# Performance work log

Hardware: AMD Instinct MI355X
Metric: run time of the kernel (lower is better)

The kernel has to match this reference:

```python
import jax, jax.numpy as jnp
import numpy as np

HEADS = 16
HEAD_DIM = 64  # embed_size 1024 // 16


def setup_inputs() -> dict:
    key = jax.random.key(0)
    ks = jax.random.split(key, 6)
    N, S, E = 2, 2048, 1024
    return {
        "values": jax.random.normal(ks[0], (N, S, E), dtype=jnp.float32),
        "keys": jax.random.normal(ks[1], (N, S, E), dtype=jnp.float32),
        "queries": jax.random.normal(ks[2], (N, S, E), dtype=jnp.float32),
        "Wv": jax.random.normal(ks[3], (E, E), dtype=jnp.float32) * (E ** -0.5),
        "Wk": jax.random.normal(ks[4], (E, E), dtype=jnp.float32) * (E ** -0.5),
        "Wq": jax.random.normal(ks[5], (E, E), dtype=jnp.float32) * (E ** -0.5),
    }


def reference(values, keys, queries, Wv, Wk, Wq):
    N, Sq, E = queries.shape
    Sk = keys.shape[1]
    H, D = HEADS, HEAD_DIM
    # linear projections (torch Linear: x @ W^T), then split heads
    v = (values @ Wv.T).reshape(N, Sk, H, D)
    k = (keys @ Wk.T).reshape(N, Sk, H, D)
    q = (queries @ Wq.T).reshape(N, Sq, H, D)
    # QK^T -> [N, H, Q, K]
    scores = jnp.einsum("nqhd,nkhd->nhqk", q, k)
    # no mask (original forward takes mask=None path); scale by sqrt(head_dim)
    attn = jax.nn.softmax(scores / jnp.asarray(D, scores.dtype) ** 0.5, axis=-1)
    # AV -> [N, Q, H, D] -> [N, Q, E]; note: fc_out is never applied in the original forward
    out = jnp.einsum("nhql,nlhd->nqhd", attn, v).reshape(N, Sq, H * D)
    return out
```

## Files before the change

kernel.cpp:

```cpp
#include <hip/hip_runtime.h>
#include <math.h>

#define SEQ 2048
#define EMB 1024
#define NH  16
#define HD  64

typedef __attribute__((ext_vector_type(8))) short short8;
typedef __attribute__((ext_vector_type(4))) float f32x4;

static const size_t XE = (size_t)2 * SEQ * EMB;
static const size_t WE = (size_t)EMB * EMB;

static __device__ __forceinline__ short f2bf(float f) {
    unsigned u = __builtin_bit_cast(unsigned, f);
    u = u + 0x7fffu + ((u >> 16) & 1u);
    return (short)(u >> 16);
}

#if __has_builtin(__builtin_amdgcn_cvt_pk_bf16_f32)
typedef __attribute__((ext_vector_type(2))) __bf16 bf16x2;
static __device__ __forceinline__ unsigned pk2(float a, float b) {
    bf16x2 v = __builtin_amdgcn_cvt_pk_bf16_f32(a, b);
    return __builtin_bit_cast(unsigned, v);
}
#else
static __device__ __forceinline__ unsigned pk2(float a, float b) {
    return (unsigned)(unsigned short)f2bf(a) |
           ((unsigned)(unsigned short)f2bf(b) << 16);
}
#endif

static __device__ __forceinline__ short8 cvt8(float4 a, float4 b) {
    union { unsigned u[4]; short8 s; } r;
    r.u[0] = pk2(a.x, a.y); r.u[1] = pk2(a.z, a.w);
    r.u[2] = pk2(b.x, b.y); r.u[3] = pk2(b.z, b.w);
    return r.s;
}

static __device__ __forceinline__ void gload16(const void* g, void* l) {
    __builtin_amdgcn_global_load_lds(
        (const __attribute__((address_space(1))) void*)g,
        (__attribute__((address_space(3))) void*)l, 16, 0, 0);
}

__global__ __launch_bounds__(256)
void cvt_all(const float* __restrict__ xq, const float* __restrict__ xk,
             const float* __restrict__ xv, const float* __restrict__ wq,
             const float* __restrict__ wk, const float* __restrict__ wv,
             short* __restrict__ dxq, short* __restrict__ dxk,
             short* __restrict__ dxv, short* __restrict__ dw) {
    int id = blockIdx.x;
    const float* s; short* d; size_t i;
    if (id < 6144) {
        int seg = id >> 11, o = id & 2047;
        s = (seg == 0) ? xq : (seg == 1) ? xk : xv;
        d = (seg == 0) ? dxq : (seg == 1) ? dxk : dxv;
        i = (size_t)o * 256 + threadIdx.x;
    } else {
        int wid = id - 6144;
        int seg = wid >> 9, o = wid & 511;
        s = (seg == 0) ? wq : (seg == 1) ? wk : wv;
        d = dw + (size_t)seg * WE;
        i = (size_t)o * 256 + threadIdx.x;
    }
    const float4* sp = (const float4*)s;
    float4 a = sp[2 * i], b = sp[2 * i + 1];
    *(short8*)(d + i * 8) = cvt8(a, b);
}

#define ES_STRIDE 136
__global__ __launch_bounds__(512, 4)
void proj(const short* __restrict__ Xq, const short* __restrict__ Xk,
          const short* __restrict__ Xv, const short* __restrict__ Wb,
          short* __restrict__ qb, short* __restrict__ kbuf,
          short* __restrict__ vt) {
    __shared__ __align__(16) char lds_raw[65536];
    short8* Fs = (short8*)lds_raw;
    short8* Hs = (short8*)(lds_raw + 32768);
    short*  Es = (short*)lds_raw;

    const int L = blockIdx.x;
    const int xcd = L & 7, i = L >> 3;
    const int z = i >> 5;
    const int m = i & 31;
    const int ty = xcd * 4 + (m & 3);
    const int tx = m >> 2;

    const short* Fop; const short* Hop; short* C;
    if (z == 0)      { Fop = Xq; Hop = Wb;           C = qb;   }
    else if (z == 1) { Fop = Xk; Hop = Wb + WE;      C = kbuf; }
    else             { Fop = Xv; Hop = Wb + 2 * WE;  C = vt;   }
    const int fr0 = ty * 128;
    const int hr0 = tx * 128;

    const int t = threadIdx.x, w = t >> 6, lane = t & 63;
    const int l15 = lane & 15, quad = lane >> 4;
    const int lr3 = lane >> 3, lc7 = lane & 7;
    const int mh = (w >> 2) * 64;
    const int nh = (w & 3) * 32;

    auto stageF = [&](int pp, int k0) {
#pragma unroll
        for (int j = 0; j < 2; ++j) {
            int rb = j * 64 + w * 8;
            gload16(Fop + (size_t)(fr0 + rb + lr3) * EMB + k0 + ((lc7 ^ lr3) * 8),
                    &Fs[pp * 1024 + rb * 8]);
        }
    };
    auto stageH = [&](int pp, int k0) {
#pragma unroll
        for (int j = 0; j < 2; ++j) {
            int rb = j * 64 + w * 8;
            gload16(Hop + (size_t)(hr0 + rb + lr3) * EMB + k0 + ((lc7 ^ lr3) * 8),
                    &Hs[pp * 1024 + rb * 8]);
        }
    };

    f32x4 acc[4][2];
#pragma unroll
    for (int a = 0; a < 4; ++a)
#pragma unroll
        for (int b = 0; b < 2; ++b) acc[a][b] = 0.f;

    stageF(0, 0);
    stageH(0, 0);

    int p = 0;
    for (int k0 = 0; k0 < EMB; k0 += 64, p ^= 1) {
        __syncthreads();
        if (k0 + 64 < EMB) { stageF(p ^ 1, k0 + 64); stageH(p ^ 1, k0 + 64); }

#pragma unroll
        for (int kb2 = 0; kb2 < 2; ++kb2) {
            short8 af[4], bf[2];
            int cx = (kb2 * 4 + quad) ^ (l15 & 7);
            if (z < 2) {
#pragma unroll
                for (int mi = 0; mi < 4; ++mi)
                    af[mi] = Fs[p * 1024 + (mh + mi * 16 + l15) * 8 + cx];
#pragma unroll
                for (int ni = 0; ni < 2; ++ni)
                    bf[ni] = Hs[p * 1024 + (nh + ni * 16 + l15) * 8 + cx];
            } else {
#pragma unroll
                for (int mi = 0; mi < 4; ++mi)
                    af[mi] = Hs[p * 1024 + (mh + mi * 16 + l15) * 8 + cx];
#pragma unroll
                for (int ni = 0; ni < 2; ++ni)
                    bf[ni] = Fs[p * 1024 + (nh + ni * 16 + l15) * 8 + cx];
            }
#pragma unroll
            for (int mi = 0; mi < 4; ++mi)
#pragma unroll
                for (int ni = 0; ni < 2; ++ni)
                    acc[mi][ni] = __builtin_amdgcn_mfma_f32_16x16x32_bf16(
                        af[mi], bf[ni], acc[mi][ni], 0, 0, 0);
        }
    }

    __syncthreads();
#pragma unroll
    for (int mi = 0; mi < 4; ++mi)
#pragma unroll
        for (int ni = 0; ni < 2; ++ni)
#pragma unroll
            for (int r = 0; r < 4; ++r) {
                int lr_ = mh + mi * 16 + quad * 4 + r;
                int lc_ = nh + ni * 16 + l15;
                Es[lr_ * ES_STRIDE + lc_] = f2bf(acc[mi][ni][r]);
            }
    __syncthreads();
    {
        int row = t >> 2, q4 = t & 3;
        const short* src = Es + row * ES_STRIDE + q4 * 32;
        short* dst;
        if (z < 2) {
            dst = C + (size_t)(fr0 + row) * EMB + hr0 + q4 * 32;
        } else {
            int bz = fr0 >> 11, s0 = fr0 & 2047;
            dst = C + ((size_t)bz * EMB + hr0 + row) * SEQ + s0 + q4 * 32;
        }
#pragma unroll
        for (int j = 0; j < 4; ++j)
            *(short8*)(dst + j * 8) = *(const short8*)(src + j * 8);
    }
}

__global__ __launch_bounds__(256, 2)
void attn_mfma(const short* __restrict__ Qg, const short* __restrict__ Kg,
               const short* __restrict__ Vtg, float* __restrict__ OutD) {
    __shared__ short8 QPs[1024];
    __shared__ short8 Ks[2][1024];
    __shared__ short8 Vs[2][1024];

    const int t = threadIdx.x, w = t >> 6, lane = t & 63;
    const int l15 = lane & 15, quad = lane >> 4;
    const int lr3 = lane >> 3, lc7 = lane & 7;
    const int L = blockIdx.x;
    const int xcd = L & 7, i = L >> 3;
    const int bh = xcd * 4 + (i & 3);
    const int q0 = (i >> 2) * 128;
    const int b = bh >> 4, h = bh & 15;
    const short* Qb = Qg + (size_t)b * SEQ * EMB + h * HD;
    const short* Kb = Kg + (size_t)b * SEQ * EMB + h * HD;
    const short* Vb = Vtg + ((size_t)b * EMB + h * HD) * SEQ;

    auto stageKV = [&](int p, int kt) {
#pragma unroll
        for (int j = 0; j < 4; ++j) {
            int rb = w * 32 + j * 8;
            int krow = rb + lr3;
            gload16(Kb + (size_t)(kt + krow) * EMB + ((lc7 ^ (krow & 7)) * 8),
                    &Ks[p][rb * 8]);
            int half = w >> 1, db = (w & 1) * 32 + j * 8;
            int d = db + lr3;
            gload16(Vb + (size_t)d * SEQ + kt + half * 64 + ((lc7 ^ (d & 7)) * 8),
                    &Vs[p][half * 512 + db * 8]);
        }
    };

#pragma unroll
    for (int j = 0; j < 4; ++j) {
        int rb = w * 32 + j * 8;
        int row = rb + lr3;
        gload16(Qb + (size_t)(q0 + row) * EMB + ((lc7 ^ (row & 7)) * 8),
                &QPs[rb * 8]);
    }
    stageKV(0, 0);
    __syncthreads();

    short8 qf[2][2];
#pragma unroll
    for (int qi = 0; qi < 2; ++qi)
#pragma unroll
        for (int kb2 = 0; kb2 < 2; ++kb2) {
            int row = w * 32 + qi * 16 + l15;
            qf[qi][kb2] = QPs[row * 8 + ((kb2 * 4 + quad) ^ (l15 & 7))];
        }

    f32x4 o[2][4];
    float lr[2] = {0.f, 0.f};
#pragma unroll
    for (int qi = 0; qi < 2; ++qi)
#pragma unroll
        for (int ni = 0; ni < 4; ++ni) o[qi][ni] = 0.f;
    const float cl2 = 0.18033688011112042f;
    const float c0  = 11.541560327111707f;

    int p = 0;
    for (int kt = 0; kt < SEQ; kt += 128, p ^= 1) {
        if (kt) __syncthreads();
        if (kt + 128 < SEQ) stageKV(p ^ 1, kt + 128);

#pragma unroll
        for (int half = 0; half < 2; ++half) {
            f32x4 s[4][2];
#pragma unroll
            for (int kblk = 0; kblk < 4; ++kblk)
#pragma unroll
                for (int qi = 0; qi < 2; ++qi) s[kblk][qi] = 0.f;
#pragma unroll
            for (int kb2 = 0; kb2 < 2; ++kb2) {
                short8 ak[4];
#pragma unroll
                for (int kblk = 0; kblk < 4; ++kblk) {
                    int row = half * 64 + kblk * 16 + l15;
                    ak[kblk] = Ks[p][row * 8 + ((kb2 * 4 + quad) ^ (l15 & 7))];
                }
#pragma unroll
                for (int kblk = 0; kblk < 4; ++kblk)
#pragma unroll
                    for (int qi = 0; qi < 2; ++qi)
                        s[kblk][qi] = __builtin_amdgcn_mfma_f32_16x16x32_bf16(
                            ak[kblk], qf[qi][kb2], s[kblk][qi], 0, 0, 0);
            }

#pragma unroll
            for (int qi = 0; qi < 2; ++qi) {
                int row = w * 32 + qi * 16 + l15;
#pragma unroll
                for (int kblk = 0; kblk < 4; ++kblk) {
                    float p0 = __builtin_amdgcn_exp2f(fmaf(s[kblk][qi][0], cl2, -c0));
                    float p1 = __builtin_amdgcn_exp2f(fmaf(s[kblk][qi][1], cl2, -c0));
                    float p2 = __builtin_amdgcn_exp2f(fmaf(s[kblk][qi][2], cl2, -c0));
                    float p3 = __builtin_amdgcn_exp2f(fmaf(s[kblk][qi][3], cl2, -c0));
                    lr[qi] += (p0 + p1) + (p2 + p3);
                    uint2 pv; pv.x = pk2(p0, p1); pv.y = pk2(p2, p3);
                    int kc = kblk * 2 + (quad >> 1);
                    *(uint2*)((char*)QPs +
                        (((row * 8 + (kc ^ (l15 & 7))) << 4) | ((quad & 1) << 3)))
                        = pv;
                }
            }

#pragma unroll
            for (int kb2 = 0; kb2 < 2; ++kb2) {
                short8 ap[2], bv[4];
#pragma unroll
                for (int qi = 0; qi < 2; ++qi) {
                    int row = w * 32 + qi * 16 + l15;
                    ap[qi] = QPs[row * 8 + ((kb2 * 4 + quad) ^ (l15 & 7))];
                }
#pragma unroll
                for (int ni = 0; ni < 4; ++ni) {
                    int dr = ni * 16 + l15;
                    bv[ni] = Vs[p][half * 512 + dr * 8 +
                                   ((kb2 * 4 + quad) ^ (l15 & 7))];
                }
#pragma unroll
                for (int qi = 0; qi < 2; ++qi)
#pragma unroll
                    for (int ni = 0; ni < 4; ++ni)
                        o[qi][ni] = __builtin_amdgcn_mfma_f32_16x16x32_bf16(
                            ap[qi], bv[ni], o[qi][ni], 0, 0, 0);
            }
        }
    }

#pragma unroll
    for (int qi = 0; qi < 2; ++qi) {
        float l = lr[qi];
        l += __shfl_xor(l, 16);
        l += __shfl_xor(l, 32);
        lr[qi] = l;
    }
#pragma unroll
    for (int qi = 0; qi < 2; ++qi)
#pragma unroll
        for (int r = 0; r < 4; ++r) {
            float inv = 1.0f / __shfl(lr[qi], quad * 4 + r);
            int q = q0 + w * 32 + qi * 16 + quad * 4 + r;
            float* op = OutD + ((size_t)b * SEQ + q) * EMB + h * HD;
#pragma unroll
            for (int ni = 0; ni < 4; ++ni)
                op[ni * 16 + l15] = o[qi][ni][r] * inv;
        }
}

extern "C" void kernel_launch(void* const* d_in, const int* in_sizes, int n_in,
                              void* d_out, int out_size, void* d_ws, size_t ws_size,
                              hipStream_t stream) {
    const float* values  = (const float*)d_in[0];
    const float* keys    = (const float*)d_in[1];
    const float* queries = (const float*)d_in[2];
    const float* Wv      = (const float*)d_in[3];
    const float* Wk      = (const float*)d_in[4];
    const float* Wq      = (const float*)d_in[5];
    float* out = (float*)d_out;

    short* qb  = (short*)d_ws;
    short* kb  = qb + XE;
    short* vt  = kb + XE;
    short* wb  = vt + XE;
    short* xqb = wb + 3 * WE;
    short* xkb = xqb + XE;
    short* xvb = xkb + XE;

    cvt_all<<<7680, 256, 0, stream>>>(queries, keys, values, Wq, Wk, Wv,
                                      xqb, xkb, xvb, wb);
    proj<<<768, 512, 0, stream>>>(xqb, xkb, xvb, wb, qb, kb, vt);
    attn_mfma<<<512, 256, 0, stream>>>(qb, kb, vt, out);
}
```

Measured before the change: 188.9 us.

## Use 8 waves of 16 query rows with 64-key tiles in attention

Restructures the attention kernel to 512-thread blocks where each wave handles 16 query rows instead of 32, and shrinks the K/V tile from 128 to 64 keys, halving shared memory. This is meant to cut register and LDS footprint, raising occupancy and latency hiding. In exchange each K/V fragment loaded from LDS feeds half as many MFMAs, and there are twice as many barriers per key sequence.

```diff
diff --git a/kernel.cpp b/kernel.cpp
--- a/kernel.cpp
+++ b/kernel.cpp
@@ -187,12 +187,12 @@
     }
 }
 
-__global__ __launch_bounds__(256, 2)
+__global__ __launch_bounds__(512, 4)
 void attn_mfma(const short* __restrict__ Qg, const short* __restrict__ Kg,
                const short* __restrict__ Vtg, float* __restrict__ OutD) {
     __shared__ short8 QPs[1024];
-    __shared__ short8 Ks[2][1024];
-    __shared__ short8 Vs[2][1024];
+    __shared__ short8 Ks[2][512];
+    __shared__ short8 Vs[2][512];
 
     const int t = threadIdx.x, w = t >> 6, lane = t & 63;
     const int l15 = lane & 15, quad = lane >> 4;
@@ -207,135 +207,104 @@
     const short* Vb = Vtg + ((size_t)b * EMB + h * HD) * SEQ;
 
     auto stageKV = [&](int p, int kt) {
-#pragma unroll
-        for (int j = 0; j < 4; ++j) {
-            int rb = w * 32 + j * 8;
-            int krow = rb + lr3;
-            gload16(Kb + (size_t)(kt + krow) * EMB + ((lc7 ^ (krow & 7)) * 8),
-                    &Ks[p][rb * 8]);
-            int half = w >> 1, db = (w & 1) * 32 + j * 8;
-            int d = db + lr3;
-            gload16(Vb + (size_t)d * SEQ + kt + half * 64 + ((lc7 ^ (d & 7)) * 8),
-                    &Vs[p][half * 512 + db * 8]);
-        }
+        int krow = w * 8 + lr3;
+        gload16(Kb + (size_t)(kt + krow) * EMB + ((lc7 ^ lr3) * 8),
+                &Ks[p][w * 64]);
+        gload16(Vb + (size_t)krow * SEQ + kt + ((lc7 ^ lr3) * 8),
+                &Vs[p][w * 64]);
     };
 
 #pragma unroll
-    for (int j = 0; j < 4; ++j) {
-        int rb = w * 32 + j * 8;
+    for (int j = 0; j < 2; ++j) {
+        int rb = w * 16 + j * 8;
         int row = rb + lr3;
-        gload16(Qb + (size_t)(q0 + row) * EMB + ((lc7 ^ (row & 7)) * 8),
+        gload16(Qb + (size_t)(q0 + row) * EMB + ((lc7 ^ lr3) * 8),
                 &QPs[rb * 8]);
     }
     stageKV(0, 0);
     __syncthreads();
 
-    short8 qf[2][2];
-#pragma unroll
-    for (int qi = 0; qi < 2; ++qi)
-#pragma unroll
-        for (int kb2 = 0; kb2 < 2; ++kb2) {
-            int row = w * 32 + qi * 16 + l15;
-            qf[qi][kb2] = QPs[row * 8 + ((kb2 * 4 + quad) ^ (l15 & 7))];
-        }
-
-    f32x4 o[2][4];
-    float lr[2] = {0.f, 0.f};
-#pragma unroll
-    for (int qi = 0; qi < 2; ++qi)
-#pragma unroll
-        for (int ni = 0; ni < 4; ++ni) o[qi][ni] = 0.f;
+    short8 qf[2];
+#pragma unroll
+    for (int kb2 = 0; kb2 < 2; ++kb2) {
+        int row = w * 16 + l15;
+        qf[kb2] = QPs[row * 8 + ((kb2 * 4 + quad) ^ (l15 & 7))];
+    }
+
+    f32x4 o[4];
+    float lr = 0.f;
+#pragma unroll
+    for (int ni = 0; ni < 4; ++ni) o[ni] = 0.f;
     const float cl2 = 0.18033688011112042f;
     const float c0  = 11.541560327111707f;
 
     int p = 0;
-    for (int kt = 0; kt < SEQ; kt += 128, p ^= 1) {
+    for (int kt = 0; kt < SEQ; kt += 64, p ^= 1) {
         if (kt) __syncthreads();
-        if (kt + 128 < SEQ) stageKV(p ^ 1, kt + 128);
-
-#pragma unroll
-        for (int half = 0; half < 2; ++half) {
-            f32x4 s[4][2];
+        if (kt + 64 < SEQ) stageKV(p ^ 1, kt + 64);
+
+        f32x4 s[4];
+#pragma unroll
+        for (int kblk = 0; kblk < 4; ++kblk) s[kblk] = 0.f;
+#pragma unroll
+        for (int kb2 = 0; kb2 < 2; ++kb2) {
+            short8 ak[4];
+#pragma unroll
+            for (int kblk = 0; kblk < 4; ++kblk) {
+                int row = kblk * 16 + l15;
+                ak[kblk] = Ks[p][row * 8 + ((kb2 * 4 + quad) ^ (l15 & 7))];
+            }
 #pragma unroll
             for (int kblk = 0; kblk < 4; ++kblk)
-#pragma unroll
-                for (int qi = 0; qi < 2; ++qi) s[kblk][qi] = 0.f;
-#pragma unroll
-            for (int kb2 = 0; kb2 < 2; ++kb2) {
-                short8 ak[4];
-#pragma unroll
-                for (int kblk = 0; kblk < 4; ++kblk) {
-                    int row = half * 64 + kblk * 16 + l15;
-                    ak[kblk] = Ks[p][row * 8 + ((kb2 * 4 + quad) ^ (l15 & 7))];
-                }
-#pragma unroll
-                for (int kblk = 0; kblk < 4; ++kblk)
-#pragma unroll
-                    for (int qi = 0; qi < 2; ++qi)
-                        s[kblk][qi] = __builtin_amdgcn_mfma_f32_16x16x32_bf16(
-                            ak[kblk], qf[qi][kb2], s[kblk][qi], 0, 0, 0);
-            }
-
-#pragma unroll
-            for (int qi = 0; qi < 2; ++qi) {
-                int row = w * 32 + qi * 16 + l15;
-#pragma unroll
-                for (int kblk = 0; kblk < 4; ++kblk) {
-                    float p0 = __builtin_amdgcn_exp2f(fmaf(s[kblk][qi][0], cl2, -c0));
-                    float p1 = __builtin_amdgcn_exp2f(fmaf(s[kblk][qi][1], cl2, -c0));
-                    float p2 = __builtin_amdgcn_exp2f(fmaf(s[kblk][qi][2], cl2, -c0));
-                    float p3 = __builtin_amdgcn_exp2f(fmaf(s[kblk][qi][3], cl2, -c0));
-                    lr[qi] += (p0 + p1) + (p2 + p3);
-                    uint2 pv; pv.x = pk2(p0, p1); pv.y = pk2(p2, p3);
-                    int kc = kblk * 2 + (quad >> 1);
-                    *(uint2*)((char*)QPs +
-                        (((row * 8 + (kc ^ (l15 & 7))) << 4) | ((quad & 1) << 3)))
-                        = pv;
-                }
-            }
-
-#pragma unroll
-            for (int kb2 = 0; kb2 < 2; ++kb2) {
-                short8 ap[2], bv[4];
-#pragma unroll
-                for (int qi = 0; qi < 2; ++qi) {
-                    int row = w * 32 + qi * 16 + l15;
-                    ap[qi] = QPs[row * 8 + ((kb2 * 4 + quad) ^ (l15 & 7))];
-                }
-#pragma unroll
-                for (int ni = 0; ni < 4; ++ni) {
-                    int dr = ni * 16 + l15;
-                    bv[ni] = Vs[p][half * 512 + dr * 8 +
-                                   ((kb2 * 4 + quad) ^ (l15 & 7))];
-                }
-#pragma unroll
-                for (int qi = 0; qi < 2; ++qi)
-#pragma unroll
-                    for (int ni = 0; ni < 4; ++ni)
-                        o[qi][ni] = __builtin_amdgcn_mfma_f32_16x16x32_bf16(
-                            ap[qi], bv[ni], o[qi][ni], 0, 0, 0);
-            }
-        }
-    }
-
-#pragma unroll
-    for (int qi = 0; qi < 2; ++qi) {
-        float l = lr[qi];
-        l += __shfl_xor(l, 16);
-        l += __shfl_xor(l, 32);
-        lr[qi] = l;
-    }
-#pragma unroll
-    for (int qi = 0; qi < 2; ++qi)
-#pragma unroll
-        for (int r = 0; r < 4; ++r) {
-            float inv = 1.0f / __shfl(lr[qi], quad * 4 + r);
-            int q = q0 + w * 32 + qi * 16 + quad * 4 + r;
-            float* op = OutD + ((size_t)b * SEQ + q) * EMB + h * HD;
+                s[kblk] = __builtin_amdgcn_mfma_f32_16x16x32_bf16(
+                    ak[kblk], qf[kb2], s[kblk], 0, 0, 0);
+        }
+
+        {
+            int row = w * 16 + l15;
+#pragma unroll
+            for (int kblk = 0; kblk < 4; ++kblk) {
+                float p0 = __builtin_amdgcn_exp2f(fmaf(s[kblk][0], cl2, -c0));
+                float p1 = __builtin_amdgcn_exp2f(fmaf(s[kblk][1], cl2, -c0));
+                float p2 = __builtin_amdgcn_exp2f(fmaf(s[kblk][2], cl2, -c0));
+                float p3 = __builtin_amdgcn_exp2f(fmaf(s[kblk][3], cl2, -c0));
+                lr += (p0 + p1) + (p2 + p3);
+                uint2 pv; pv.x = pk2(p0, p1); pv.y = pk2(p2, p3);
+                int kc = kblk * 2 + (quad >> 1);
+                *(uint2*)((char*)QPs +
+                    (((row * 8 + (kc ^ (l15 & 7))) << 4) | ((quad & 1) << 3)))
+                    = pv;
+            }
+        }
+
+#pragma unroll
+        for (int kb2 = 0; kb2 < 2; ++kb2) {
+            int row = w * 16 + l15;
+            short8 ap = QPs[row * 8 + ((kb2 * 4 + quad) ^ (l15 & 7))];
+            short8 bv[4];
+#pragma unroll
+            for (int ni = 0; ni < 4; ++ni) {
+                int dr = ni * 16 + l15;
+                bv[ni] = Vs[p][dr * 8 + ((kb2 * 4 + quad) ^ (l15 & 7))];
+            }
 #pragma unroll
             for (int ni = 0; ni < 4; ++ni)
-                op[ni * 16 + l15] = o[qi][ni][r] * inv;
-        }
+                o[ni] = __builtin_amdgcn_mfma_f32_16x16x32_bf16(
+                    ap, bv[ni], o[ni], 0, 0, 0);
+        }
+    }
+
+    lr += __shfl_xor(lr, 16);
+    lr += __shfl_xor(lr, 32);
+#pragma unroll
+    for (int r = 0; r < 4; ++r) {
+        float inv = 1.0f / __shfl(lr, quad * 4 + r);
+        int q = q0 + w * 16 + quad * 4 + r;
+        float* op = OutD + ((size_t)b * SEQ + q) * EMB + h * HD;
+#pragma unroll
+        for (int ni = 0; ni < 4; ++ni)
+            op[ni * 16 + l15] = o[ni][r] * inv;
+    }
 }
 
 extern "C" void kernel_launch(void* const* d_in, const int* in_sizes, int n_in,
@@ -360,5 +329,5 @@
     cvt_all<<<7680, 256, 0, stream>>>(queries, keys, values, Wq, Wk, Wv,
                                       xqb, xkb, xvb, wb);
     proj<<<768, 512, 0, stream>>>(xqb, xkb, xvb, wb, qb, kb, vt);
-    attn_mfma<<<512, 256, 0, stream>>>(qb, kb, vt, out);
-}
+    attn_mfma<<<512, 512, 0, stream>>>(qb, kb, vt, out);
+}
```

After: 200.2 us. +6.0%, slower.

## Use triple-buffered 64-key tiles with partial vmcnt waits and one barrier

Applied to the files above, without the earlier changes.

Shrinks the K/V tile from 128 to 64 keys and triple-buffers it, prefetching two tiles ahead. The full __syncthreads is replaced by an s_waitcnt vmcnt(4) plus a raw s_barrier, so the next tile's loads can still be in flight while the current one is computed. MFMA blocks are wrapped in s_setprio to favour matrix issue. This adds more loop iterations and barriers, and its correctness relies on the exact count of outstanding loads per stage.

```diff
diff --git a/kernel.cpp b/kernel.cpp
--- a/kernel.cpp
+++ b/kernel.cpp
@@ -191,8 +191,8 @@
 void attn_mfma(const short* __restrict__ Qg, const short* __restrict__ Kg,
                const short* __restrict__ Vtg, float* __restrict__ OutD) {
     __shared__ short8 QPs[1024];
-    __shared__ short8 Ks[2][1024];
-    __shared__ short8 Vs[2][1024];
+    __shared__ short8 Ks[3][512];
+    __shared__ short8 Vs[3][512];
 
     const int t = threadIdx.x, w = t >> 6, lane = t & 63;
     const int l15 = lane & 15, quad = lane >> 4;
@@ -208,27 +208,27 @@
 
     auto stageKV = [&](int p, int kt) {
 #pragma unroll
-        for (int j = 0; j < 4; ++j) {
-            int rb = w * 32 + j * 8;
-            int krow = rb + lr3;
-            gload16(Kb + (size_t)(kt + krow) * EMB + ((lc7 ^ (krow & 7)) * 8),
+        for (int j = 0; j < 2; ++j) {
+            int rb = w * 16 + j * 8;
+            int r = rb + lr3;
+            gload16(Kb + (size_t)(kt + r) * EMB + ((lc7 ^ lr3) * 8),
                     &Ks[p][rb * 8]);
-            int half = w >> 1, db = (w & 1) * 32 + j * 8;
-            int d = db + lr3;
-            gload16(Vb + (size_t)d * SEQ + kt + half * 64 + ((lc7 ^ (d & 7)) * 8),
-                    &Vs[p][half * 512 + db * 8]);
+            gload16(Vb + (size_t)r * SEQ + kt + ((lc7 ^ lr3) * 8),
+                    &Vs[p][rb * 8]);
         }
     };
 
 #pragma unroll
     for (int j = 0; j < 4; ++j) {
         int rb = w * 32 + j * 8;
-        int row = rb + lr3;
-        gload16(Qb + (size_t)(q0 + row) * EMB + ((lc7 ^ (row & 7)) * 8),
+        gload16(Qb + (size_t)(q0 + rb + lr3) * EMB + ((lc7 ^ lr3) * 8),
                 &QPs[rb * 8]);
     }
     stageKV(0, 0);
-    __syncthreads();
+    stageKV(1, 64);
+    asm volatile("s_waitcnt vmcnt(4)" ::: "memory");
+    __builtin_amdgcn_s_barrier();
+    __builtin_amdgcn_sched_barrier(0);
 
     short8 qf[2][2];
 #pragma unroll
@@ -249,73 +249,86 @@
     const float c0  = 11.541560327111707f;
 
     int p = 0;
-    for (int kt = 0; kt < SEQ; kt += 128, p ^= 1) {
-        if (kt) __syncthreads();
-        if (kt + 128 < SEQ) stageKV(p ^ 1, kt + 128);
-
-#pragma unroll
-        for (int half = 0; half < 2; ++half) {
-            f32x4 s[4][2];
+    for (int kt = 0; kt < SEQ; kt += 64) {
+        if (kt) {
+            if (kt + 64 < SEQ) {
+                asm volatile("s_waitcnt vmcnt(4)" ::: "memory");
+            } else {
+                asm volatile("s_waitcnt vmcnt(0)" ::: "memory");
+            }
+            __builtin_amdgcn_s_barrier();
+            __builtin_amdgcn_sched_barrier(0);
+        }
+        if (kt + 128 < SEQ) {
+            int pn = p + 2; if (pn >= 3) pn -= 3;
+            stageKV(pn, kt + 128);
+        }
+
+        f32x4 s[4][2];
+#pragma unroll
+        for (int kblk = 0; kblk < 4; ++kblk)
+#pragma unroll
+            for (int qi = 0; qi < 2; ++qi) s[kblk][qi] = 0.f;
+#pragma unroll
+        for (int kb2 = 0; kb2 < 2; ++kb2) {
+            short8 ak[4];
+#pragma unroll
+            for (int kblk = 0; kblk < 4; ++kblk) {
+                int row = kblk * 16 + l15;
+                ak[kblk] = Ks[p][row * 8 + ((kb2 * 4 + quad) ^ (l15 & 7))];
+            }
+            __builtin_amdgcn_s_setprio(1);
 #pragma unroll
             for (int kblk = 0; kblk < 4; ++kblk)
 #pragma unroll
-                for (int qi = 0; qi < 2; ++qi) s[kblk][qi] = 0.f;
-#pragma unroll
-            for (int kb2 = 0; kb2 < 2; ++kb2) {
-                short8 ak[4];
-#pragma unroll
-                for (int kblk = 0; kblk < 4; ++kblk) {
-                    int row = half * 64 + kblk * 16 + l15;
-                    ak[kblk] = Ks[p][row * 8 + ((kb2 * 4 + quad) ^ (l15 & 7))];
-                }
-#pragma unroll
-                for (int kblk = 0; kblk < 4; ++kblk)
-#pragma unroll
-                    for (int qi = 0; qi < 2; ++qi)
-                        s[kblk][qi] = __builtin_amdgcn_mfma_f32_16x16x32_bf16(
-                            ak[kblk], qf[qi][kb2], s[kblk][qi], 0, 0, 0);
-            }
-
+                for (int qi = 0; qi < 2; ++qi)
+                    s[kblk][qi] = __builtin_amdgcn_mfma_f32_16x16x32_bf16(
+                        ak[kblk], qf[qi][kb2], s[kblk][qi], 0, 0, 0);
+            __builtin_amdgcn_s_setprio(0);
+        }
+
+#pragma unroll
+        for (int qi = 0; qi < 2; ++qi) {
+            int row = w * 32 + qi * 16 + l15;
+#pragma unroll
+            for (int kblk = 0; kblk < 4; ++kblk) {
+                float p0 = __builtin_amdgcn_exp2f(fmaf(s[kblk][qi][0], cl2, -c0));
+                float p1 = __builtin_amdgcn_exp2f(fmaf(s[kblk][qi][1], cl2, -c0));
+                float p2 = __builtin_amdgcn_exp2f(fmaf(s[kblk][qi][2], cl2, -c0));
+                float p3 = __builtin_amdgcn_exp2f(fmaf(s[kblk][qi][3], cl2, -c0));
+                lr[qi] += (p0 + p1) + (p2 + p3);
+                uint2 pv; pv.x = pk2(p0, p1); pv.y = pk2(p2, p3);
+                int kc = kblk * 2 + (quad >> 1);
+                *(uint2*)((char*)QPs +
+                    (((row * 8 + (kc ^ (l15 & 7))) << 4) | ((quad & 1) << 3)))
+                    = pv;
+            }
+        }
+
+#pragma unroll
+        for (int kb2 = 0; kb2 < 2; ++kb2) {
+            short8 ap[2], bv[4];
 #pragma unroll
             for (int qi = 0; qi < 2; ++qi) {
                 int row = w * 32 + qi * 16 + l15;
-#pragma unroll
-                for (int kblk = 0; kblk < 4; ++kblk) {
-                    float p0 = __builtin_amdgcn_exp2f(fmaf(s[kblk][qi][0], cl2, -c0));
-                    float p1 = __builtin_amdgcn_exp2f(fmaf(s[kblk][qi][1], cl2, -c0));
-                    float p2 = __builtin_amdgcn_exp2f(fmaf(s[kblk][qi][2], cl2, -c0));
-                    float p3 = __builtin_amdgcn_exp2f(fmaf(s[kblk][qi][3], cl2, -c0));
-                    lr[qi] += (p0 + p1) + (p2 + p3);
-                    uint2 pv; pv.x = pk2(p0, p1); pv.y = pk2(p2, p3);
-                    int kc = kblk * 2 + (quad >> 1);
-                    *(uint2*)((char*)QPs +
-                        (((row * 8 + (kc ^ (l15 & 7))) << 4) | ((quad & 1) << 3)))
-                        = pv;
-                }
-            }
-
-#pragma unroll
-            for (int kb2 = 0; kb2 < 2; ++kb2) {
-                short8 ap[2], bv[4];
-#pragma unroll
-                for (int qi = 0; qi < 2; ++qi) {
-                    int row = w * 32 + qi * 16 + l15;
-                    ap[qi] = QPs[row * 8 + ((kb2 * 4 + quad) ^ (l15 & 7))];
-                }
-#pragma unroll
-                for (int ni = 0; ni < 4; ++ni) {
-                    int dr = ni * 16 + l15;
-                    bv[ni] = Vs[p][half * 512 + dr * 8 +
-                                   ((kb2 * 4 + quad) ^ (l15 & 7))];
-                }
-#pragma unroll
-                for (int qi = 0; qi < 2; ++qi)
-#pragma unroll
-                    for (int ni = 0; ni < 4; ++ni)
-                        o[qi][ni] = __builtin_amdgcn_mfma_f32_16x16x32_bf16(
-                            ap[qi], bv[ni], o[qi][ni], 0, 0, 0);
-            }
-        }
+                ap[qi] = QPs[row * 8 + ((kb2 * 4 + quad) ^ (l15 & 7))];
+            }
+#pragma unroll
+            for (int ni = 0; ni < 4; ++ni) {
+                int dr = ni * 16 + l15;
+                bv[ni] = Vs[p][dr * 8 + ((kb2 * 4 + quad) ^ (l15 & 7))];
+            }
+            __builtin_amdgcn_s_setprio(1);
+#pragma unroll
+            for (int qi = 0; qi < 2; ++qi)
+#pragma unroll
+                for (int ni = 0; ni < 4; ++ni)
+                    o[qi][ni] = __builtin_amdgcn_mfma_f32_16x16x32_bf16(
+                        ap[qi], bv[ni], o[qi][ni], 0, 0, 0);
+            __builtin_amdgcn_s_setprio(0);
+        }
+
+        p = (p + 1 == 3) ? 0 : p + 1;
     }
 
 #pragma unroll
```

Result: no change. 192.1 us (+1.7%).
